# Kernel tuning notes

Hardware: AMD Instinct MI355X
Metric: run time of the kernel (lower is better)

The kernel has to match this reference:

```python
import jax, jax.numpy as jnp
import numpy as np

STRIDE, PADDING, EPS = 2, 1, 1e-5


def setup_inputs() -> dict:
    key = jax.random.key(0)
    k1, k2, k3 = jax.random.split(key, 3)
    C_in, C_out, K = 64, 64, 4
    x = jax.random.normal(k1, (32, C_in, 64, 64), dtype=jnp.float32)
    weight = jax.random.normal(k2, (C_in, C_out, K, K), dtype=jnp.float32) * 0.05  # torch layout (in,out,kh,kw)
    conv_bias = jax.random.normal(k3, (C_out,), dtype=jnp.float32) * 0.02
    gamma = jnp.ones((C_out,), dtype=jnp.float32)
    beta = jnp.zeros((C_out,), dtype=jnp.float32)
    running_mean = jnp.zeros((C_out,), dtype=jnp.float32)
    running_var = jnp.ones((C_out,), dtype=jnp.float32)
    return {"x": x, "weight": weight, "conv_bias": conv_bias, "gamma": gamma,
            "beta": beta, "running_mean": running_mean, "running_var": running_var}


def _conv_transpose2d(x, weight, bias, stride, padding):
    # torch.nn.functional.conv_transpose2d equivalent:
    # conv with lhs_dilation=stride, spatially-flipped kernel, in/out axes swapped,
    # and padding k-1-p on each side.
    k = weight.shape[2]
    w_t = jnp.transpose(jnp.flip(weight, (2, 3)), (1, 0, 2, 3))  # (Cout, Cin, k, k)
    pad = k - 1 - padding
    y = jax.lax.conv_general_dilated(
        x, w_t,
        window_strides=(1, 1),
        padding=[(pad, pad), (pad, pad)],
        lhs_dilation=(stride, stride),
        dimension_numbers=("NCHW", "OIHW", "NCHW"),
    )
    return y + bias[None, :, None, None]


def reference(x, weight, conv_bias, gamma, beta, running_mean, running_var):
    # ConvTranspose2d
    y = _conv_transpose2d(x, weight, conv_bias, STRIDE, PADDING)  # [N,C,128,128]
    # BatchNorm2d (inference, running stats)
    scale = gamma * jax.lax.rsqrt(running_var + EPS)
    y = (y - running_mean[None, :, None, None]) * scale[None, :, None, None] + beta[None, :, None, None]
    # Softmax over channel dim
    y = jax.nn.softmax(y, axis=1)
    # MaxPool2d(k=2, s=2): H,W are even, so reshape-max is exact
    N, C, H, W = y.shape
    y = y.reshape(N, C, H // 2, 2, W // 2, 2).max(axis=(3, 5))  # [N,C,64,64]
    return y
```

## Files before the change

### kernel.cpp

```cpp
#include <hip/hip_runtime.h>
#include <hip/hip_bf16.h>
#include <math.h>


typedef __attribute__((ext_vector_type(8))) short short8;
typedef __attribute__((ext_vector_type(4))) float floatx4;
typedef __attribute__((ext_vector_type(2))) unsigned uint2v;

__device__ ushort g_wfrag[4 * 8 * 4 * 64 * 8];
__device__ float g_aff[64];

#define L2E 1.44269504088896340736f

__device__ __forceinline__ ushort f2bf(float f) {
  union { float f; unsigned u; } v; v.f = f;
  unsigned r = v.u + 0x7FFF + ((v.u >> 16) & 1);
  return (ushort)(r >> 16);
}

__global__ __launch_bounds__(256) void prep_kernel(
    const float* __restrict__ w, const float* __restrict__ bias,
    const float* __restrict__ gamma, const float* __restrict__ beta,
    const float* __restrict__ mean, const float* __restrict__ var) {
  int t = blockIdx.x * 256 + threadIdx.x;
  int cin0 = (t >> 6) * 2;
  int cout = t & 63;
  int nt = cout >> 4, b15 = cout & 15;
  int q = (cin0 & 31) >> 3;
  int j = cin0 & 7;
  int ksq = cin0 >> 5;
  float Aw = gamma[cout] * rsqrtf(var[cout] + 1e-5f) * L2E;

  const float4* p0 = (const float4*)&w[(cin0 * 64 + cout) * 16];
  const float4* p1 = (const float4*)&w[((cin0 + 1) * 64 + cout) * 16];
  float a[16], b[16];
  {
    float4 f0 = p0[0], f1 = p0[1], f2 = p0[2], f3 = p0[3];
    a[0]=f0.x; a[1]=f0.y; a[2]=f0.z; a[3]=f0.w; a[4]=f1.x; a[5]=f1.y; a[6]=f1.z; a[7]=f1.w;
    a[8]=f2.x; a[9]=f2.y; a[10]=f2.z; a[11]=f2.w; a[12]=f3.x; a[13]=f3.y; a[14]=f3.z; a[15]=f3.w;
    float4 g0 = p1[0], g1 = p1[1], g2 = p1[2], g3 = p1[3];
    b[0]=g0.x; b[1]=g0.y; b[2]=g0.z; b[3]=g0.w; b[4]=g1.x; b[5]=g1.y; b[6]=g1.z; b[7]=g1.w;
    b[8]=g2.x; b[9]=g2.y; b[10]=g2.z; b[11]=g2.w; b[12]=g3.x; b[13]=g3.y; b[14]=g3.z; b[15]=g3.w;
  }
#pragma unroll
  for (int kh = 0; kh < 4; ++kh)
#pragma unroll
    for (int kw = 0; kw < 4; ++kw) {
      int r = (kh & 1) ? 0 : 1;
      int pp = (kw & 1) ? 0 : 1;
      int c = r * 2 + pp;
      int tap = (kh >> 1) * 2 + (kw >> 1);
      int ks = tap * 2 + ksq;
      unsigned u = (unsigned)f2bf(a[kh * 4 + kw] * Aw) |
                   ((unsigned)f2bf(b[kh * 4 + kw] * Aw) << 16);
      *(unsigned*)&g_wfrag[(((c * 8 + ks) * 4 + nt) * 64 + q * 16 + b15) * 8 + j] = u;
    }

  if (t < 64) {
    float A0 = gamma[t] * rsqrtf(var[t] + 1e-5f);
    g_aff[t] = ((bias[t] - mean[t]) * A0 + beta[t]) * L2E;
  }
}

__device__ __forceinline__ unsigned cvtpk(float a, float b) {
  unsigned r;
  asm("v_cvt_pk_bf16_f32 %0, %1, %2" : "=v"(r) : "v"(a), "v"(b));
  return r;
}

template <int CTRL>
__device__ __forceinline__ float dpp_add(float v) {
  unsigned t = (unsigned)__builtin_amdgcn_update_dpp(
      0, (int)__float_as_uint(v), CTRL, 0xF, 0xF, true);
  return v + __uint_as_float(t);
}

__device__ __forceinline__ float sum16(float v) {
  v = dpp_add<0xB1>(v);
  v = dpp_add<0x4E>(v);
  v = dpp_add<0x141>(v);
  v = dpp_add<0x140>(v);
  return v;
}

__device__ __forceinline__ float fexp2(float x) {
#if __has_builtin(__builtin_amdgcn_exp2f)
  return __builtin_amdgcn_exp2f(x);
#else
  return exp2f(x);
#endif
}

__device__ __forceinline__ void gload_lds16(const void* g, void* l) {
  __builtin_amdgcn_global_load_lds(
      (const __attribute__((address_space(1))) void*)g,
      (__attribute__((address_space(3))) void*)l, 16, 0, 0);
}

#define COLS 66
#define ROWSTRIDE (COLS * 64)

__global__ __launch_bounds__(512, 2) void fused_kernel(const float* __restrict__ x,
                                                       float* __restrict__ out) {
  __shared__ __align__(16) ushort xs[4 * ROWSTRIDE];
  __shared__ __align__(16) ushort wbuf[2 * 8 * 4 * 512];
  __shared__ __align__(16) float red[2 * 64 * 65 + 16];

  const int tid  = threadIdx.x;
  const int swz  = ((blockIdx.x & 7) << 2) | (blockIdx.x >> 3);
  const int ph0  = swz * 2;
  const int n    = blockIdx.y;
  const int wave = tid >> 6;
  const int lane = tid & 63;
  const int b15  = lane & 15;
  const int q    = lane >> 4;
  const int wc   = wave & 1;
  const int c    = wave >> 1;
  const int r    = c >> 1, p = c & 1;

#define STAGE_W(buf_, ks_)                                                    \
  {                                                                           \
    _Pragma("unroll")                                                         \
    for (int nt_ = 0; nt_ < 4; ++nt_)                                         \
      gload_lds16(&g_wfrag[(((c * 8 + (ks_)) * 4 + nt_) * 64 + lane) * 8],    \
                  &wbuf[(((buf_)*8 + wave) * 4 + nt_) * 512]);                \
  }
  STAGE_W(0, 0);

  {
    float4 z = {0.f, 0.f, 0.f, 0.f};
    for (int e = tid; e < 2084; e += 512) ((float4*)red)[e] = z;
  }

  for (int e = tid; e < 1024; e += 512) {
    int iw4 = e & 15;
    int c4  = (e >> 4) & 15;
    int row = e >> 8;
    int ih  = ph0 - 1 + row;
    float4 v0 = {0.f, 0.f, 0.f, 0.f}, v1 = v0, v2 = v0, v3 = v0;
    if (ih >= 0 && ih < 64) {
      const float* xp = x + ((n * 64 + c4 * 4) * 64 + ih) * 64 + iw4 * 4;
      v0 = *(const float4*)xp;          v1 = *(const float4*)(xp + 4096);
      v2 = *(const float4*)(xp + 8192); v3 = *(const float4*)(xp + 12288);
    }
    int chunk = c4 >> 1, half4 = (c4 & 1) * 4;
    float cc[4][4] = {{v0.x, v1.x, v2.x, v3.x}, {v0.y, v1.y, v2.y, v3.y},
                      {v0.z, v1.z, v2.z, v3.z}, {v0.w, v1.w, v2.w, v3.w}};
#pragma unroll
    for (int ii = 0; ii < 4; ++ii) {
      int col = iw4 * 4 + ii + 1;
      uint2v pk = {cvtpk(cc[ii][0], cc[ii][1]), cvtpk(cc[ii][2], cc[ii][3])};
      *(uint2v*)&xs[(row * COLS + col) * 64 + ((chunk ^ (col & 7)) * 8) + half4] = pk;
    }
  }
  for (int e = tid; e < 128; e += 512) {
    int c4 = e & 15, side = (e >> 4) & 1, row = e >> 5;
    int col = side ? 65 : 0;
    int chunk = c4 >> 1, half4 = (c4 & 1) * 4;
    ushort4 z; z.x = z.y = z.z = z.w = 0;
    *(ushort4*)&xs[(row * COLS + col) * 64 + ((chunk ^ (col & 7)) * 8) + half4] = z;
  }

  float Dc[4];
#pragma unroll
  for (int nt = 0; nt < 4; ++nt) Dc[nt] = g_aff[nt * 16 + b15];

  int A2[2][2];
#pragma unroll
  for (int b = 0; b < 2; ++b) {
    int col = wc * 32 + b15 + (b ? p - 1 : p) + 1;
#pragma unroll
    for (int par = 0; par < 2; ++par)
      A2[b][par] = r * ROWSTRIDE + col * 64 + (((par * 4 + q) ^ (col & 7)) * 8);
  }

  __syncthreads();

  floatx4 acc[16];
#pragma unroll
  for (int i = 0; i < 16; ++i) {
    float d = Dc[i & 3];
    acc[i] = (floatx4){d, d, d, d};
  }

#pragma unroll
  for (int ks = 0; ks < 8; ++ks) {
    const int cur = ks & 1;
    asm volatile("s_waitcnt vmcnt(0)" ::: "memory");
    short8 bf[4];
#pragma unroll
    for (int nt = 0; nt < 4; ++nt)
      bf[nt] = *(const short8*)&wbuf[((cur * 8 + wave) * 4 + nt) * 512 + lane * 8];
    const int b_ = (ks >> 1) & 1, par_ = ks & 1;
    const int ro = (ks >> 2) ? 0 : ROWSTRIDE;
    const int base = A2[b_][par_] + ro;
    short8 af00 = *(const short8*)&xs[base];
    short8 af01 = *(const short8*)&xs[base + 1024];
    short8 af10 = *(const short8*)&xs[base + ROWSTRIDE];
    short8 af11 = *(const short8*)&xs[base + ROWSTRIDE + 1024];
    if (ks < 7) STAGE_W(cur ^ 1, ks + 1);
#pragma unroll
    for (int nt = 0; nt < 4; ++nt) {
      acc[nt]      = __builtin_amdgcn_mfma_f32_16x16x32_bf16(af00, bf[nt], acc[nt], 0, 0, 0);
      acc[4 + nt]  = __builtin_amdgcn_mfma_f32_16x16x32_bf16(af01, bf[nt], acc[4 + nt], 0, 0, 0);
      acc[8 + nt]  = __builtin_amdgcn_mfma_f32_16x16x32_bf16(af10, bf[nt], acc[8 + nt], 0, 0, 0);
      acc[12 + nt] = __builtin_amdgcn_mfma_f32_16x16x32_bf16(af11, bf[nt], acc[12 + nt], 0, 0, 0);
    }
  }

#pragma unroll
  for (int prow = 0; prow < 2; ++prow)
#pragma unroll
    for (int mt = 0; mt < 2; ++mt) {
      float sm[4] = {0.f, 0.f, 0.f, 0.f};
#pragma unroll
      for (int nt = 0; nt < 4; ++nt)
#pragma unroll
        for (int reg = 0; reg < 4; ++reg) {
          float e = fexp2(acc[prow * 8 + mt * 4 + nt][reg]);
          acc[prow * 8 + mt * 4 + nt][reg] = e;
          sm[reg] += e;
        }
#pragma unroll
      for (int reg = 0; reg < 4; ++reg)
        sm[reg] = __builtin_amdgcn_rcpf(sum16(sm[reg]));
#pragma unroll
      for (int nt = 0; nt < 4; ++nt) {
        int idx = (prow * 64 + nt * 16 + b15) * 65 + wc * 32 + mt * 16 + q * 4;
#pragma unroll
        for (int reg = 0; reg < 4; ++reg) {
          float v = acc[prow * 8 + mt * 4 + nt][reg] * sm[reg];
          __hip_atomic_fetch_max((unsigned*)&red[idx + reg], __float_as_uint(v),
                                 __ATOMIC_RELAXED, __HIP_MEMORY_SCOPE_WORKGROUP);
        }
      }
    }
  __syncthreads();

  for (int e = tid; e < 4096; e += 512) {
    int pw2  = e & 31;
    int cout = (e >> 5) & 63;
    int rl   = e >> 11;
    int base = (rl * 64 + cout) * 65 + pw2 * 2;
    float2 val = {red[base], red[base + 1]};
    *(float2*)&out[((n * 64 + cout) * 64 + (ph0 + rl)) * 64 + pw2 * 2] = val;
  }
}

extern "C" void kernel_launch(void* const* d_in, const int* in_sizes, int n_in,
                              void* d_out, int out_size, void* d_ws, size_t ws_size,
                              hipStream_t stream) {
  const float* x     = (const float*)d_in[0];
  const float* w     = (const float*)d_in[1];
  const float* bias  = (const float*)d_in[2];
  const float* gamma = (const float*)d_in[3];
  const float* beta  = (const float*)d_in[4];
  const float* mean  = (const float*)d_in[5];
  const float* var   = (const float*)d_in[6];
  float* out = (float*)d_out;

  prep_kernel<<<8, 256, 0, stream>>>(w, bias, gamma, beta, mean, var);
  dim3 grid(32, 32);
  fused_kernel<<<grid, 512, 0, stream>>>(x, out);
}
```

Measured before the change: 117.8 us.

## Alias weight buffer into reduction LDS, single-buffer weights, raise occupancy bound

The double-buffered weight staging area is removed, and a single weight buffer now aliases the reduction scratch array. This cuts LDS use per block and lets launch_bounds request 4 blocks per CU instead of 2. To keep this correct, the weight prefetch now waits on all LDS reads before overwriting the buffer. The reduction also changes: the zero-fill is dropped, one quarter of the waves write their values directly, and the rest then apply atomic max. The trade-off is less overlap between the weight prefetch and compute, an extra barrier, and tighter register limits at the higher occupancy target.

```diff
diff --git a/kernel.cpp b/kernel.cpp
--- a/kernel.cpp
+++ b/kernel.cpp
@@ -100,11 +100,12 @@
 #define COLS 66
 #define ROWSTRIDE (COLS * 64)
 
-__global__ __launch_bounds__(512, 2) void fused_kernel(const float* __restrict__ x,
+__global__ __launch_bounds__(512, 4) void fused_kernel(const float* __restrict__ x,
                                                        float* __restrict__ out) {
   __shared__ __align__(16) ushort xs[4 * ROWSTRIDE];
-  __shared__ __align__(16) ushort wbuf[2 * 8 * 4 * 512];
   __shared__ __align__(16) float red[2 * 64 * 65 + 16];
+
+  ushort* wbuf = (ushort*)red;
 
   const int tid  = threadIdx.x;
   const int swz  = ((blockIdx.x & 7) << 2) | (blockIdx.x >> 3);
@@ -118,19 +119,14 @@
   const int c    = wave >> 1;
   const int r    = c >> 1, p = c & 1;
 
-#define STAGE_W(buf_, ks_)                                                    \
+#define STAGE_W(ks_)                                                          \
   {                                                                           \
     _Pragma("unroll")                                                         \
     for (int nt_ = 0; nt_ < 4; ++nt_)                                         \
       gload_lds16(&g_wfrag[(((c * 8 + (ks_)) * 4 + nt_) * 64 + lane) * 8],    \
-                  &wbuf[(((buf_)*8 + wave) * 4 + nt_) * 512]);                \
-  }
-  STAGE_W(0, 0);
-
-  {
-    float4 z = {0.f, 0.f, 0.f, 0.f};
-    for (int e = tid; e < 2084; e += 512) ((float4*)red)[e] = z;
-  }
+                  &wbuf[(wave * 4 + nt_) * 512]);                             \
+  }
+  STAGE_W(0);
 
   for (int e = tid; e < 1024; e += 512) {
     int iw4 = e & 15;
@@ -185,12 +181,11 @@
 
 #pragma unroll
   for (int ks = 0; ks < 8; ++ks) {
-    const int cur = ks & 1;
     asm volatile("s_waitcnt vmcnt(0)" ::: "memory");
     short8 bf[4];
 #pragma unroll
     for (int nt = 0; nt < 4; ++nt)
-      bf[nt] = *(const short8*)&wbuf[((cur * 8 + wave) * 4 + nt) * 512 + lane * 8];
+      bf[nt] = *(const short8*)&wbuf[(wave * 4 + nt) * 512 + lane * 8];
     const int b_ = (ks >> 1) & 1, par_ = ks & 1;
     const int ro = (ks >> 2) ? 0 : ROWSTRIDE;
     const int base = A2[b_][par_] + ro;
@@ -198,7 +193,8 @@
     short8 af01 = *(const short8*)&xs[base + 1024];
     short8 af10 = *(const short8*)&xs[base + ROWSTRIDE];
     short8 af11 = *(const short8*)&xs[base + ROWSTRIDE + 1024];
-    if (ks < 7) STAGE_W(cur ^ 1, ks + 1);
+    asm volatile("s_waitcnt lgkmcnt(0)" ::: "memory");
+    if (ks < 7) STAGE_W(ks + 1);
 #pragma unroll
     for (int nt = 0; nt < 4; ++nt) {
       acc[nt]      = __builtin_amdgcn_mfma_f32_16x16x32_bf16(af00, bf[nt], acc[nt], 0, 0, 0);
@@ -225,16 +221,43 @@
       for (int reg = 0; reg < 4; ++reg)
         sm[reg] = __builtin_amdgcn_rcpf(sum16(sm[reg]));
 #pragma unroll
-      for (int nt = 0; nt < 4; ++nt) {
-        int idx = (prow * 64 + nt * 16 + b15) * 65 + wc * 32 + mt * 16 + q * 4;
-#pragma unroll
-        for (int reg = 0; reg < 4; ++reg) {
-          float v = acc[prow * 8 + mt * 4 + nt][reg] * sm[reg];
-          __hip_atomic_fetch_max((unsigned*)&red[idx + reg], __float_as_uint(v),
-                                 __ATOMIC_RELAXED, __HIP_MEMORY_SCOPE_WORKGROUP);
+      for (int nt = 0; nt < 4; ++nt)
+#pragma unroll
+        for (int reg = 0; reg < 4; ++reg)
+          acc[prow * 8 + mt * 4 + nt][reg] *= sm[reg];
+    }
+
+  __syncthreads();
+
+  if (c == 0) {
+#pragma unroll
+    for (int prow = 0; prow < 2; ++prow)
+#pragma unroll
+      for (int mt = 0; mt < 2; ++mt)
+#pragma unroll
+        for (int nt = 0; nt < 4; ++nt) {
+          int idx = (prow * 64 + nt * 16 + b15) * 65 + wc * 32 + mt * 16 + q * 4;
+#pragma unroll
+          for (int reg = 0; reg < 4; ++reg)
+            red[idx + reg] = acc[prow * 8 + mt * 4 + nt][reg];
         }
-      }
-    }
+  }
+  __syncthreads();
+  if (c != 0) {
+#pragma unroll
+    for (int prow = 0; prow < 2; ++prow)
+#pragma unroll
+      for (int mt = 0; mt < 2; ++mt)
+#pragma unroll
+        for (int nt = 0; nt < 4; ++nt) {
+          int idx = (prow * 64 + nt * 16 + b15) * 65 + wc * 32 + mt * 16 + q * 4;
+#pragma unroll
+          for (int reg = 0; reg < 4; ++reg)
+            __hip_atomic_fetch_max((unsigned*)&red[idx + reg],
+                                   __float_as_uint(acc[prow * 8 + mt * 4 + nt][reg]),
+                                   __ATOMIC_RELAXED, __HIP_MEMORY_SCOPE_WORKGROUP);
+        }
+  }
   __syncthreads();
 
   for (int e = tid; e < 4096; e += 512) {
```

New measurement: 113.3 us. 1.04x faster.
